# Performance work log

Measured on AMD Instinct MI355X. Metric: run time of the kernel, lower is better.

The kernel has to match this reference:

```python
import jax, jax.numpy as jnp
import numpy as np

D_MODEL = 4096
N_HEADS = 32
KV_HEADS = 8
HEAD_DIM = D_MODEL // N_HEADS  # 128
GROUPS = N_HEADS // KV_HEADS   # 4
ROPE_THETA = 500000.0
CLIP_QKV = 8.0
SEQLENS = [512, 768, 384, 384]
T = sum(SEQLENS)  # 2048 total ragged tokens


def setup_inputs() -> dict:
    key = jax.random.key(0)
    k1, k2, k3 = jax.random.split(key, 3)
    hidden_states = jax.random.normal(k1, (T, D_MODEL), dtype=jnp.float32)
    # fused Wqkv: rows = d_model (Q) + 2 * kv_heads * head_dim (K,V)
    w_qkv = jax.random.normal(k2, (D_MODEL + 2 * KV_HEADS * HEAD_DIM, D_MODEL), dtype=jnp.float32) * 0.02
    w_o = jax.random.normal(k3, (D_MODEL, D_MODEL), dtype=jnp.float32) * 0.02
    # ragged-batch metadata: cumulative sequence lengths, per-token positions
    cu = np.concatenate([[0], np.cumsum(SEQLENS)]).astype(np.int32)
    pos = np.concatenate([np.arange(l) for l in SEQLENS]).astype(np.float32)
    inv_freq = 1.0 / (ROPE_THETA ** (np.arange(0, HEAD_DIM, 2, dtype=np.float32) / HEAD_DIM))  # [64]
    freqs = pos[:, None] * inv_freq[None, :]  # [T, 64]
    return {
        "hidden_states": hidden_states,
        "w_qkv": w_qkv,
        "w_o": w_o,
        "cos": jnp.asarray(np.cos(freqs), dtype=jnp.float32),
        "sin": jnp.asarray(np.sin(freqs), dtype=jnp.float32),
        "cu_seqlens": jnp.asarray(cu),
    }


def _rope(x, cos, sin):
    # rotate-half (NeoX-style) RoPE, as in TGI PositionRotaryEmbedding
    h = HEAD_DIM // 2
    x1, x2 = x[..., :h], x[..., h:]
    c = cos[:, None, :]  # [T,1,h] broadcast over heads
    s = sin[:, None, :]
    return jnp.concatenate([x1 * c - x2 * s, x2 * c + x1 * s], axis=-1)


def reference(hidden_states, w_qkv, w_o, cos, sin, cu_seqlens):
    # fused QKV projection + clip_qkv clamp
    qkv = jnp.clip(hidden_states @ w_qkv.T, -CLIP_QKV, CLIP_QKV)  # [T, 6144]
    q_sz = N_HEADS * HEAD_DIM
    kv_sz = KV_HEADS * HEAD_DIM
    q = qkv[:, :q_sz].reshape(T, N_HEADS, HEAD_DIM)
    k = qkv[:, q_sz:q_sz + kv_sz].reshape(T, KV_HEADS, HEAD_DIM)
    v = qkv[:, q_sz + kv_sz:].reshape(T, KV_HEADS, HEAD_DIM)
    q = _rope(q, cos, sin)
    k = _rope(k, cos, sin)
    # GQA: expand kv heads to query heads (kv_head_mapping = repeat_interleave)
    kr = jnp.repeat(k, GROUPS, axis=1)  # [T, H, D]
    vr = jnp.repeat(v, GROUPS, axis=1)
    # varlen causal mask: same segment AND key index <= query index
    idx = jnp.arange(T)
    seg = jnp.searchsorted(cu_seqlens, idx, side="right") - 1  # [T]
    mask = (seg[:, None] == seg[None, :]) & (idx[:, None] >= idx[None, :])  # [T,T]
    scale = HEAD_DIM ** -0.5
    scores = jnp.einsum("qhd,khd->hqk", q, kr) * scale  # [H,T,T]
    scores = jnp.where(mask[None, :, :], scores, jnp.finfo(scores.dtype).min)
    attn = jax.nn.softmax(scores, axis=-1)
    out = jnp.einsum("hqk,khd->qhd", attn, vr).reshape(T, N_HEADS * HEAD_DIM)
    return out @ w_o.T
```

## Files before the change

### kernel.cpp

```cpp
#include <hip/hip_runtime.h>

#define T_TOK 2048
#define DM    4096
#define NH    32
#define KVH   8
#define HD    128
#define QKV_N 6144
#define KOFF  4096
#define VOFF  5120
#define SCALE 0.08838834764831845f

typedef __attribute__((ext_vector_type(8))) short  short8;
typedef __attribute__((ext_vector_type(4))) float  floatx4;

__device__ __forceinline__ ushort f2bf(float f) {
  union { float f; unsigned u; } x; x.f = f;
  unsigned u = x.u;
  return (ushort)((u + 0x7fffu + ((u >> 16) & 1u)) >> 16);
}
__device__ __forceinline__ float bf2f(ushort h) {
  union { unsigned u; float f; } x; x.u = ((unsigned)h) << 16;
  return x.f;
}

__global__ void __launch_bounds__(256) cast_bf16_kernel(const float* __restrict__ x,
                                                        ushort* __restrict__ y, int n4) {
  int i = blockIdx.x * 256 + threadIdx.x;
  if (i >= n4) return;
  float4 v = ((const float4*)x)[i];
  ushort4 o;
  o.x = f2bf(v.x); o.y = f2bf(v.y); o.z = f2bf(v.z); o.w = f2bf(v.w);
  ((ushort4*)y)[i] = o;
}

__device__ __forceinline__ void gld_lds16(const ushort* g, ushort* l) {
  __builtin_amdgcn_global_load_lds((const __attribute__((address_space(1))) unsigned int*)g,
                                   (__attribute__((address_space(3))) unsigned int*)l,
                                   16, 0, 0);
}

__device__ __forceinline__ void bar() {
  asm volatile("" ::: "memory");
  __builtin_amdgcn_s_barrier();
  asm volatile("" ::: "memory");
}

template <int MLO, int NLO>
__device__ __forceinline__ void mfma_quad(floatx4 (&acc)[8][4],
                                          const short8 (&afr)[4][2],
                                          const short8 (&bfr)[4][2]) {
  __builtin_amdgcn_s_setprio(1);
#pragma unroll
  for (int ks = 0; ks < 2; ++ks)
#pragma unroll
    for (int mi = 0; mi < 4; ++mi)
#pragma unroll
      for (int ni = 0; ni < 2; ++ni)
        acc[MLO + mi][NLO + ni] = __builtin_amdgcn_mfma_f32_16x16x32_bf16(
            afr[mi][ks], bfr[NLO + ni][ks], acc[MLO + mi][NLO + ni], 0, 0, 0);
  __builtin_amdgcn_s_setprio(0);
}

__device__ __forceinline__ void stage_half(const ushort* __restrict__ G, size_t row0,
                                           int K, int k0, ushort* lbase, int tid) {
#pragma unroll
  for (int j = 0; j < 2; ++j) {
    int row   = j * 64 + (tid >> 3);
    int chunk = (tid & 7) ^ (row & 7);
    gld_lds16(G + (row0 + (size_t)row) * K + k0 + chunk * 8,
              lbase + (size_t)(j * 512 + tid) * 8);
  }
}

__global__ void __launch_bounds__(512, 2)
gemm256(const ushort* __restrict__ A, const ushort* __restrict__ B,
        ushort* __restrict__ Cb, float* __restrict__ Cf, int N, int K, int mode) {
  __shared__ __align__(16) ushort As[2][2][128][64];
  __shared__ __align__(16) ushort Bs[2][2][128][64];

  const int tid = threadIdx.x;
  const int lane = tid & 63, wv = tid >> 6;
  const int r = lane & 15, g = lane >> 4;
  const int wm = wv >> 2, wn = wv & 3;

  const int nwg = (int)gridDim.x;
  const int wg  = (int)blockIdx.x;
  const int wgs = (wg & 7) * (nwg >> 3) + (wg >> 3);
  const int nbx = N >> 8;
  const int bx = wgs % nbx, by = wgs / nbx;
  const int bm = by * 256, bn = bx * 256;

  const int NT = K >> 6;

  floatx4 acc[8][4];
#pragma unroll
  for (int mi = 0; mi < 8; ++mi)
#pragma unroll
    for (int ni = 0; ni < 4; ++ni) acc[mi][ni] = (floatx4){0.f, 0.f, 0.f, 0.f};

  stage_half(B, bn,       K, 0, &Bs[0][0][0][0], tid);
  stage_half(B, bn + 128, K, 0, &Bs[0][1][0][0], tid);
  stage_half(A, bm,       K, 0, &As[0][0][0][0], tid);
  stage_half(A, bm + 128, K, 0, &As[0][1][0][0], tid);
  if (NT > 1) {
    stage_half(B, bn,       K, 64, &Bs[1][0][0][0], tid);
    stage_half(B, bn + 128, K, 64, &Bs[1][1][0][0], tid);
    stage_half(A, bm,       K, 64, &As[1][0][0][0], tid);
    asm volatile("s_waitcnt vmcnt(6)" ::: "memory");
  } else {
    asm volatile("s_waitcnt vmcnt(0)" ::: "memory");
  }
  bar();

  short8 afr[4][2], bfr[4][2];
  const int cswz = (r & 7) << 3;

  for (int t = 0; t < NT; ++t) {
    const int buf = t & 1;
    const ushort* Ab = &As[buf][wm][0][0];
    const ushort* Bb = &Bs[buf][wn >> 1][0][0];
    const int brow = (wn & 1) * 64;

#pragma unroll
    for (int ni = 0; ni < 4; ++ni)
#pragma unroll
      for (int ks = 0; ks < 2; ++ks)
        bfr[ni][ks] = *(const short8*)&Bb[(brow + ni * 16 + r) * 64 +
                                          ((ks * 32 + g * 8) ^ cswz)];
#pragma unroll
    for (int m = 0; m < 4; ++m)
#pragma unroll
      for (int ks = 0; ks < 2; ++ks)
        afr[m][ks] = *(const short8*)&Ab[(m * 16 + r) * 64 +
                                         ((ks * 32 + g * 8) ^ cswz)];
    if (t + 1 < NT) stage_half(A, bm + 128, K, (t + 1) * 64, &As[(t + 1) & 1][1][0][0], tid);
    asm volatile("s_waitcnt lgkmcnt(0)" ::: "memory");
    bar();
    mfma_quad<0, 0>(acc, afr, bfr);
    bar();

    if (t + 2 < NT) stage_half(B, bn, K, (t + 2) * 64, &Bs[buf][0][0][0], tid);
    bar();
    mfma_quad<0, 2>(acc, afr, bfr);
    bar();

#pragma unroll
    for (int m = 0; m < 4; ++m)
#pragma unroll
      for (int ks = 0; ks < 2; ++ks)
        afr[m][ks] = *(const short8*)&Ab[((64 + m * 16) + r) * 64 +
                                         ((ks * 32 + g * 8) ^ cswz)];
    if (t + 2 < NT) stage_half(B, bn + 128, K, (t + 2) * 64, &Bs[buf][1][0][0], tid);
    asm volatile("s_waitcnt lgkmcnt(0)" ::: "memory");
    bar();
    mfma_quad<4, 2>(acc, afr, bfr);
    bar();

    if (t + 2 < NT) stage_half(A, bm, K, (t + 2) * 64, &As[buf][0][0][0], tid);
    if (t < NT - 2) asm volatile("s_waitcnt vmcnt(6)" ::: "memory");
    else            asm volatile("s_waitcnt vmcnt(0)" ::: "memory");
    bar();
    mfma_quad<4, 0>(acc, afr, bfr);
    bar();
  }

#pragma unroll
  for (int mi = 0; mi < 8; ++mi)
#pragma unroll
    for (int v = 0; v < 4; ++v) {
      int row = bm + wm * 128 + mi * 16 + g * 4 + v;
#pragma unroll
      for (int ni = 0; ni < 4; ++ni) {
        int col = bn + wn * 64 + ni * 16 + r;
        float x = acc[mi][ni][v];
        if (mode == 0) {
          x = fminf(8.0f, fmaxf(-8.0f, x));
          Cb[(size_t)row * N + col] = f2bf(x);
        } else {
          Cf[(size_t)row * N + col] = x;
        }
      }
    }
}

__global__ void __launch_bounds__(256) rope_kernel(ushort* __restrict__ qkv,
                                                   const float* __restrict__ cosb,
                                                   const float* __restrict__ sinb) {
  int t = blockIdx.y;
  int h = blockIdx.x * 4 + (threadIdx.x >> 6);
  int d = threadIdx.x & 63;
  size_t base = (size_t)t * QKV_N + (h < NH ? h * HD : KOFF + (h - NH) * HD);
  float x1 = bf2f(qkv[base + d]);
  float x2 = bf2f(qkv[base + 64 + d]);
  float c = cosb[t * 64 + d], s = sinb[t * 64 + d];
  float y1 = x1 * c - x2 * s;
  float y2 = x2 * c + x1 * s;
  if (h < NH) { y1 *= SCALE; y2 *= SCALE; }
  qkv[base + d]      = f2bf(y1);
  qkv[base + 64 + d] = f2bf(y2);
}

__global__ void __launch_bounds__(256) vtrans_kernel(const ushort* __restrict__ qkv,
                                                     ushort* __restrict__ vt) {
  int idx = blockIdx.x * 256 + threadIdx.x;
  int t  = idx & (T_TOK - 1);
  int d  = (idx >> 11) & (HD - 1);
  int kv = idx >> 18;
  vt[idx] = qkv[(size_t)t * QKV_N + VOFF + kv * HD + d];
}

__global__ void __launch_bounds__(256) attn_kernel(const ushort* __restrict__ qkv,
                                                   const ushort* __restrict__ vt,
                                                   ushort* __restrict__ o) {
  __shared__ ushort Ks[64][136];
  __shared__ ushort Vts[128][72];
  __shared__ ushort Ps[4][16][72];

  const int tid = threadIdx.x, wave = tid >> 6, lane = tid & 63;
  const int r = lane & 15, g = lane >> 4;
  const int qtile = blockIdx.x, head = blockIdx.y, kvh = head >> 2;
  const int q0 = qtile * 64;
  int s0;
  if (q0 < 512) s0 = 0; else if (q0 < 1280) s0 = 512;
  else if (q0 < 1664) s0 = 1280; else s0 = 1664;

  short8 qf[4];
  const int qrow = q0 + wave * 16 + r;
#pragma unroll
  for (int ks = 0; ks < 4; ks++)
    qf[ks] = *(const short8*)&qkv[(size_t)qrow * QKV_N + head * HD + ks * 32 + g * 8];

  floatx4 zero = {0.f, 0.f, 0.f, 0.f};
  floatx4 oacc[8];
#pragma unroll
  for (int b = 0; b < 8; b++) oacc[b] = zero;
  float mrun[4] = {-1e30f, -1e30f, -1e30f, -1e30f};
  float lrun[4] = {0.f, 0.f, 0.f, 0.f};

  const size_t kcol  = (size_t)KOFF + kvh * HD;
  const size_t vbase = (size_t)kvh * HD * T_TOK;

  for (int k0 = s0; k0 < q0 + 64; k0 += 64) {
    short8 kreg[4], vreg[4];
#pragma unroll
    for (int p = 0; p < 4; p++) {
      int krow = p * 16 + (tid >> 4), kc = (tid & 15) * 8;
      kreg[p] = *(const short8*)&qkv[(size_t)(k0 + krow) * QKV_N + kcol + kc];
      int vd = p * 32 + (tid >> 3), vc = (tid & 7) * 8;
      vreg[p] = *(const short8*)&vt[vbase + (size_t)vd * T_TOK + k0 + vc];
    }
    __syncthreads();
#pragma unroll
    for (int p = 0; p < 4; p++) {
      int krow = p * 16 + (tid >> 4), kc = (tid & 15) * 8;
      *(short8*)&Ks[krow][kc] = kreg[p];
      int vd = p * 32 + (tid >> 3), vc = (tid & 7) * 8;
      *(short8*)&Vts[vd][vc] = vreg[p];
    }
    __syncthreads();

    floatx4 sacc[4];
#pragma unroll
    for (int s = 0; s < 4; s++) sacc[s] = zero;
#pragma unroll
    for (int s = 0; s < 4; s++)
#pragma unroll
      for (int ks = 0; ks < 4; ks++) {
        short8 kf = *(const short8*)&Ks[s * 16 + r][ks * 32 + g * 8];
        sacc[s] = __builtin_amdgcn_mfma_f32_16x16x32_bf16(qf[ks], kf, sacc[s], 0, 0, 0);
      }

    const bool diag = (k0 == q0);
    float sv[4][4];
#pragma unroll
    for (int s = 0; s < 4; s++)
#pragma unroll
      for (int v = 0; v < 4; v++) {
        float x = sacc[s][v];
        if (diag) {
          int ka = k0 + s * 16 + r;
          int qa = q0 + wave * 16 + g * 4 + v;
          if (ka > qa) x = -1e30f;
        }
        sv[s][v] = x;
      }

    float rmax[4];
#pragma unroll
    for (int v = 0; v < 4; v++)
      rmax[v] = fmaxf(fmaxf(sv[0][v], sv[1][v]), fmaxf(sv[2][v], sv[3][v]));
#pragma unroll
    for (int off = 1; off < 16; off <<= 1)
#pragma unroll
      for (int v = 0; v < 4; v++)
        rmax[v] = fmaxf(rmax[v], __shfl_xor(rmax[v], off, 64));

    float newm[4], alpha[4];
#pragma unroll
    for (int v = 0; v < 4; v++) {
      newm[v]  = fmaxf(mrun[v], rmax[v]);
      alpha[v] = __expf(mrun[v] - newm[v]);
      mrun[v]  = newm[v];
    }

    float pv[4][4];
    float rsum[4] = {0.f, 0.f, 0.f, 0.f};
#pragma unroll
    for (int s = 0; s < 4; s++)
#pragma unroll
      for (int v = 0; v < 4; v++) {
        float p = __expf(sv[s][v] - newm[v]);
        pv[s][v] = p;
        rsum[v] += p;
      }
#pragma unroll
    for (int off = 1; off < 16; off <<= 1)
#pragma unroll
      for (int v = 0; v < 4; v++)
        rsum[v] += __shfl_xor(rsum[v], off, 64);
#pragma unroll
    for (int v = 0; v < 4; v++) lrun[v] = lrun[v] * alpha[v] + rsum[v];
#pragma unroll
    for (int b = 0; b < 8; b++)
#pragma unroll
      for (int v = 0; v < 4; v++) oacc[b][v] *= alpha[v];

#pragma unroll
    for (int s = 0; s < 4; s++)
#pragma unroll
      for (int v = 0; v < 4; v++)
        Ps[wave][g * 4 + v][s * 16 + r] = f2bf(pv[s][v]);
    __syncthreads();

    short8 pf0 = *(const short8*)&Ps[wave][r][g * 8];
    short8 pf1 = *(const short8*)&Ps[wave][r][32 + g * 8];

#pragma unroll
    for (int b = 0; b < 8; b++) {
      short8 v0 = *(const short8*)&Vts[b * 16 + r][g * 8];
      short8 v1 = *(const short8*)&Vts[b * 16 + r][32 + g * 8];
      oacc[b] = __builtin_amdgcn_mfma_f32_16x16x32_bf16(pf0, v0, oacc[b], 0, 0, 0);
      oacc[b] = __builtin_amdgcn_mfma_f32_16x16x32_bf16(pf1, v1, oacc[b], 0, 0, 0);
    }
  }

  float rinv[4];
#pragma unroll
  for (int v = 0; v < 4; v++) rinv[v] = 1.0f / lrun[v];
#pragma unroll
  for (int b = 0; b < 8; b++)
#pragma unroll
    for (int v = 0; v < 4; v++) {
      int qa = q0 + wave * 16 + g * 4 + v;
      o[(size_t)qa * DM + head * HD + b * 16 + r] = f2bf(oacc[b][v] * rinv[v]);
    }
}

extern "C" void kernel_launch(void* const* d_in, const int* in_sizes, int n_in,
                              void* d_out, int out_size, void* d_ws, size_t ws_size,
                              hipStream_t stream) {
  const float* hs   = (const float*)d_in[0];
  const float* wqkv = (const float*)d_in[1];
  const float* wo   = (const float*)d_in[2];
  const float* cosb = (const float*)d_in[3];
  const float* sinb = (const float*)d_in[4];
  float* out = (float*)d_out;

  char* w = (char*)d_ws;
  ushort* h_bf   = (ushort*)(w);
  ushort* wq_bf  = (ushort*)(w + 16777216);
  ushort* wo_bf  = (ushort*)(w + 67108864);
  ushort* qkv_bf = (ushort*)(w + 100663296);
  ushort* vt     = (ushort*)(w + 125829120);
  ushort* ao_bf  = (ushort*)(w + 130023424);

  cast_bf16_kernel<<<8192,  256, 0, stream>>>(hs,   h_bf,  2097152);
  cast_bf16_kernel<<<24576, 256, 0, stream>>>(wqkv, wq_bf, 6291456);
  cast_bf16_kernel<<<16384, 256, 0, stream>>>(wo,   wo_bf, 4194304);

  gemm256<<<dim3(192), 512, 0, stream>>>(h_bf, wq_bf, qkv_bf, nullptr, QKV_N, DM, 0);
  rope_kernel<<<dim3(10, T_TOK), 256, 0, stream>>>(qkv_bf, cosb, sinb);
  vtrans_kernel<<<8192, 256, 0, stream>>>(qkv_bf, vt);
  attn_kernel<<<dim3(32, 32), 256, 0, stream>>>(qkv_bf, vt, ao_bf);
  gemm256<<<dim3(128), 512, 0, stream>>>(ao_bf, wo_bf, nullptr, out, DM, DM, 1);
}
```

Before: 576.1 us.

## Reschedule GEMM main-loop LDS fragment loads and drop explicit memory clobbers

Reorders the GEMM K-loop so the second half of the B fragments is read from LDS just before the MFMA quad that uses it. The global→LDS stage of the next B half moves later and is merged with the next A stage. The explicit lgkmcnt(0) waits and the compiler memory clobbers around barriers and vmcnt waits are removed, which lets the compiler place its own LDS waits and interleave loads with MFMAs. The aim is more overlap of LDS reads and async global loads with matrix math. The risk is ordering bugs between the async LDS writes and reads, since the compiler no longer sees these waits as memory fences.

```diff
diff --git a/kernel.cpp b/kernel.cpp
--- a/kernel.cpp
+++ b/kernel.cpp
@@ -39,12 +39,6 @@
                                    16, 0, 0);
 }
 
-__device__ __forceinline__ void bar() {
-  asm volatile("" ::: "memory");
-  __builtin_amdgcn_s_barrier();
-  asm volatile("" ::: "memory");
-}
-
 template <int MLO, int NLO>
 __device__ __forceinline__ void mfma_quad(floatx4 (&acc)[8][4],
                                           const short8 (&afr)[4][2],
@@ -106,11 +100,11 @@
     stage_half(B, bn,       K, 64, &Bs[1][0][0][0], tid);
     stage_half(B, bn + 128, K, 64, &Bs[1][1][0][0], tid);
     stage_half(A, bm,       K, 64, &As[1][0][0][0], tid);
-    asm volatile("s_waitcnt vmcnt(6)" ::: "memory");
+    asm volatile("s_waitcnt vmcnt(6)");
   } else {
-    asm volatile("s_waitcnt vmcnt(0)" ::: "memory");
+    asm volatile("s_waitcnt vmcnt(0)");
   }
-  bar();
+  __builtin_amdgcn_s_barrier();
 
   short8 afr[4][2], bfr[4][2];
   const int cswz = (r & 7) << 3;
@@ -122,7 +116,7 @@
     const int brow = (wn & 1) * 64;
 
 #pragma unroll
-    for (int ni = 0; ni < 4; ++ni)
+    for (int ni = 0; ni < 2; ++ni)
 #pragma unroll
       for (int ks = 0; ks < 2; ++ks)
         bfr[ni][ks] = *(const short8*)&Bb[(brow + ni * 16 + r) * 64 +
@@ -134,15 +128,19 @@
         afr[m][ks] = *(const short8*)&Ab[(m * 16 + r) * 64 +
                                          ((ks * 32 + g * 8) ^ cswz)];
     if (t + 1 < NT) stage_half(A, bm + 128, K, (t + 1) * 64, &As[(t + 1) & 1][1][0][0], tid);
-    asm volatile("s_waitcnt lgkmcnt(0)" ::: "memory");
-    bar();
+    __builtin_amdgcn_s_barrier();
     mfma_quad<0, 0>(acc, afr, bfr);
-    bar();
-
-    if (t + 2 < NT) stage_half(B, bn, K, (t + 2) * 64, &Bs[buf][0][0][0], tid);
-    bar();
+    __builtin_amdgcn_s_barrier();
+
+#pragma unroll
+    for (int ni = 2; ni < 4; ++ni)
+#pragma unroll
+      for (int ks = 0; ks < 2; ++ks)
+        bfr[ni][ks] = *(const short8*)&Bb[(brow + ni * 16 + r) * 64 +
+                                          ((ks * 32 + g * 8) ^ cswz)];
+    __builtin_amdgcn_s_barrier();
     mfma_quad<0, 2>(acc, afr, bfr);
-    bar();
+    __builtin_amdgcn_s_barrier();
 
 #pragma unroll
     for (int m = 0; m < 4; ++m)
@@ -150,18 +148,20 @@
       for (int ks = 0; ks < 2; ++ks)
         afr[m][ks] = *(const short8*)&Ab[((64 + m * 16) + r) * 64 +
                                          ((ks * 32 + g * 8) ^ cswz)];
-    if (t + 2 < NT) stage_half(B, bn + 128, K, (t + 2) * 64, &Bs[buf][1][0][0], tid);
-    asm volatile("s_waitcnt lgkmcnt(0)" ::: "memory");
-    bar();
+    if (t + 2 < NT) stage_half(B, bn, K, (t + 2) * 64, &Bs[buf][0][0][0], tid);
+    __builtin_amdgcn_s_barrier();
     mfma_quad<4, 2>(acc, afr, bfr);
-    bar();
-
-    if (t + 2 < NT) stage_half(A, bm, K, (t + 2) * 64, &As[buf][0][0][0], tid);
-    if (t < NT - 2) asm volatile("s_waitcnt vmcnt(6)" ::: "memory");
-    else            asm volatile("s_waitcnt vmcnt(0)" ::: "memory");
-    bar();
+    __builtin_amdgcn_s_barrier();
+
+    if (t + 2 < NT) {
+      stage_half(B, bn + 128, K, (t + 2) * 64, &Bs[buf][1][0][0], tid);
+      stage_half(A, bm,       K, (t + 2) * 64, &As[buf][0][0][0], tid);
+    }
+    if (t < NT - 2) asm volatile("s_waitcnt vmcnt(6)");
+    else            asm volatile("s_waitcnt vmcnt(0)");
+    __builtin_amdgcn_s_barrier();
     mfma_quad<4, 0>(acc, afr, bfr);
-    bar();
+    __builtin_amdgcn_s_barrier();
   }
 
 #pragma unroll
```

Result: no change. 567.6 us (-1.5%).
